# Kernel tuning notes

Hardware: AMD Instinct MI355X
Metric: run time of the kernel (lower is better)

The kernel has to match this reference:

```python
import jax, jax.numpy as jnp
import numpy as np

B, IN, UNITS, E = 32768, 1024, 1024, 8

def setup_inputs() -> dict:
    key = jax.random.key(0)
    k1, k2, k3, k4 = jax.random.split(key, 4)
    x = jax.random.normal(k1, (B, IN), dtype=jnp.float32)
    # gate percentages: soft mixing weights over experts (sum to 1 like a softmax gate)
    gate_perc = jax.nn.softmax(jax.random.normal(k2, (B, E), dtype=jnp.float32), axis=-1)
    alpha = jax.random.normal(k3, (E, IN, UNITS), dtype=jnp.float32) * 0.05  # 'random_normal' init
    beta = jax.random.normal(k4, (E, UNITS), dtype=jnp.float32) * 0.05
    return {"x": x, "gate_perc": gate_perc, "alpha": alpha, "beta": beta}

def reference(x, gate_perc, alpha, beta):
    # Original math: w[b] = sum_e gate[b,e] * alpha[e]; bias[b] = sum_e gate[b,e] * beta[e];
    #                out = x[b] @ w[b] + bias[b]
    # Algebraically identical, avoiding the (B, IN, UNITS) per-sample weight tensor:
    # out[b,u] = sum_e gate[b,e] * (x[b] @ alpha[e])[u] + (gate @ beta)[b,u]
    out = jnp.einsum('bi,eiu,be->bu', x, alpha, gate_perc, optimize=True)
    out = out + gate_perc @ beta
    return out
```

## Files before the change

### kernel.cpp

```cpp
#include <hip/hip_runtime.h>

#define BSZ   32768
#define INF   1024
#define UNITS 1024
#define NE    8

using bf16x8 = __attribute__((ext_vector_type(8))) __bf16;
using f32x4  = __attribute__((ext_vector_type(4))) float;

#define GLD_LDS16(gp, lp)                                                        \
  __builtin_amdgcn_global_load_lds((__attribute__((address_space(1))) void*)(gp),\
                                   (__attribute__((address_space(3))) void*)(lp),\
                                   16, 0, 0)

__global__ __launch_bounds__(256) void transpose_cvt(const float* __restrict__ a,
                                                     __bf16* __restrict__ at) {
  __shared__ float tile[32][33];
  const int e  = blockIdx.z;
  const int u0 = blockIdx.x * 32;
  const int i0 = blockIdx.y * 32;
  const float* src = a  + (size_t)e * (INF * UNITS);
  __bf16*      dst = at + (size_t)e * (INF * UNITS);
  const int tx = threadIdx.x & 31, ty = threadIdx.x >> 5;
#pragma unroll
  for (int r = 0; r < 32; r += 8)
    tile[ty + r][tx] = src[(size_t)(i0 + ty + r) * UNITS + (u0 + tx)];
  __syncthreads();
#pragma unroll
  for (int r = 0; r < 32; r += 8)
    dst[(size_t)(u0 + ty + r) * INF + (i0 + tx)] = (__bf16)tile[tx][ty + r];
}

__global__ __launch_bounds__(256) void cvt_x(const float* __restrict__ x,
                                             __bf16* __restrict__ xb) {
  const size_t i = ((size_t)blockIdx.x * 256 + threadIdx.x) * 8;
  f32x4 a = *(const f32x4*)(x + i);
  f32x4 b = *(const f32x4*)(x + i + 4);
  bf16x8 h;
  h[0] = (__bf16)a.x; h[1] = (__bf16)a.y; h[2] = (__bf16)a.z; h[3] = (__bf16)a.w;
  h[4] = (__bf16)b.x; h[5] = (__bf16)b.y; h[6] = (__bf16)b.z; h[7] = (__bf16)b.w;
  *(bf16x8*)(xb + i) = h;
}

__global__ __launch_bounds__(512, 2) void gemm_kernel(
    const __bf16* __restrict__ xb, const float* __restrict__ gate,
    const __bf16* __restrict__ aT, const float* __restrict__ beta,
    float* __restrict__ out) {
  __shared__ __align__(16) __bf16 lA[4][128 * 64];
  __shared__ __align__(16) __bf16 lB[4][128 * 64];
  __shared__ float lG[256 * NE];

  const int t    = threadIdx.x;
  const int wave = t >> 6;
  const int lane = t & 63;
  const int wm   = wave >> 2;
  const int wn   = wave & 3;
  const int hB   = wn >> 1;
  const int fm   = lane & 15;
  const int kq   = lane >> 4;
  const int fq   = kq * 4;
  const int sw   = fm & 7;
  const int bR   = (wn & 1) * 64 + fm;

  const int li = (blockIdx.x & 7) * 64 + (blockIdx.x >> 3);
  const int bn = (li >> 7) * 256;
  const int bm = (li & 127) * 256;

  *(f32x4*)&lG[t * 4] = *(const f32x4*)&gate[(size_t)bm * NE + t * 4];

  const int stRow   = wave * 16 + (lane >> 3);
  const int stChunk = ((lane & 7) ^ (lane >> 3)) << 3;
  const __bf16* pA  = xb + (size_t)(bm + stRow) * INF + stChunk;
  const __bf16* pB  = aT + (size_t)(bn + stRow) * INF + stChunk;

#define STAGE_A(SLOT, KT, HF)                                                   \
  do {                                                                          \
    const __bf16* s_ = pA + (size_t)(HF) * (128 * INF) + (((KT) & 15) << 6);    \
    GLD_LDS16(s_, &lA[SLOT][(wave * 16) * 64]);                                 \
    GLD_LDS16(s_ + 8 * INF, &lA[SLOT][(wave * 16 + 8) * 64]);                   \
  } while (0)

#define STAGE_B(SLOT, KT, HF)                                                   \
  do {                                                                          \
    const __bf16* s_ = pB + ((size_t)((KT) >> 4) << 20) +                       \
                       (size_t)(HF) * (128 * INF) + (((KT) & 15) << 6);         \
    GLD_LDS16(s_, &lB[SLOT][(wave * 16) * 64]);                                 \
    GLD_LDS16(s_ + 8 * INF, &lB[SLOT][(wave * 16 + 8) * 64]);                   \
  } while (0)

#define LDAF(SLOT, ROW, C) \
  (*(const bf16x8*)&lA[SLOT][((ROW) << 6) + ((((C) ^ sw)) << 3)])
#define LDBF(SLOT, ROW, C) \
  (*(const bf16x8*)&lB[SLOT][((ROW) << 6) + ((((C) ^ sw)) << 3)])

#define LOAD_B(SLOT)                                    \
  _Pragma("unroll") for (int n = 0; n < 4; ++n) {       \
    bq[n][0] = LDBF(SLOT, bR + n * 16, kq);             \
    bq[n][1] = LDBF(SLOT, bR + n * 16, 4 + kq);         \
  }

#define LOAD_A(SLOT, Q)                                        \
  _Pragma("unroll") for (int mm = 0; mm < 2; ++mm) {           \
    aq[mm][0] = LDAF(SLOT, (Q) * 32 + mm * 16 + fm, kq);       \
    aq[mm][1] = LDAF(SLOT, (Q) * 32 + mm * 16 + fm, 4 + kq);   \
  }

#define VMW(N) asm volatile("s_waitcnt vmcnt(" #N ")" ::: "memory")

#define MFMA_BLK(Q)                                                            \
  do {                                                                         \
    __builtin_amdgcn_s_barrier();                                              \
    asm volatile("s_waitcnt lgkmcnt(0)" ::: "memory");                         \
    __builtin_amdgcn_s_setprio(1);                                             \
    _Pragma("unroll") for (int mm = 0; mm < 2; ++mm)                           \
    _Pragma("unroll") for (int n = 0; n < 4; ++n) {                            \
      acc[(Q) * 2 + mm][n] = __builtin_amdgcn_mfma_f32_16x16x32_bf16(          \
          aq[mm][0], bq[n][0], acc[(Q) * 2 + mm][n], 0, 0, 0);                 \
      acc[(Q) * 2 + mm][n] = __builtin_amdgcn_mfma_f32_16x16x32_bf16(          \
          aq[mm][1], bq[n][1], acc[(Q) * 2 + mm][n], 0, 0, 0);                 \
    }                                                                          \
    __builtin_amdgcn_s_setprio(0);                                             \
    __builtin_amdgcn_s_barrier();                                              \
    asm volatile("" ::: "memory");                                             \
  } while (0)

#define RESCALE(E)                                                 \
  do {                                                             \
    _Pragma("unroll") for (int m = 0; m < 8; ++m)                  \
    _Pragma("unroll") for (int r = 0; r < 4; ++r) {                \
      const int rowL  = wm * 128 + m * 16 + fq + r;                \
      const float go  = lG[rowL * NE + (E)-1];                     \
      const float gn  = lG[rowL * NE + (E)];                       \
      const float ra  = go / gn;                                   \
      _Pragma("unroll") for (int n = 0; n < 4; ++n)                \
        acc[m][n][r] *= ra;                                        \
    }                                                              \
  } while (0)

  bf16x8 aq[2][2], bq[4][2];
  f32x4  acc[8][4] = {};

  STAGE_B(0, 0, 0); STAGE_B(1, 0, 1);
  STAGE_A(0, 0, 0); STAGE_A(1, 0, 1);
  STAGE_B(2, 1, 0); STAGE_B(3, 1, 1);
  asm volatile("s_waitcnt vmcnt(4) lgkmcnt(0)" ::: "memory");
  __builtin_amdgcn_s_barrier();
  asm volatile("" ::: "memory");

#pragma unroll 1
  for (int i = 0; i < 63; ++i) {
    if (i && !(i & 7)) RESCALE(i >> 3);
    const int kt1 = 2 * i + 1, ktn = 2 * i + 2, ktn1 = 2 * i + 3;
    LOAD_B(hB);     LOAD_A(wm, 0);     STAGE_A(2, kt1, 0);           MFMA_BLK(0);
                    LOAD_A(wm, 1);     STAGE_A(3, kt1, 1);           MFMA_BLK(1);
                    LOAD_A(wm, 2);     STAGE_B(0, ktn, 0);           MFMA_BLK(2);
                    LOAD_A(wm, 3);     STAGE_B(1, ktn, 1);  VMW(4);  MFMA_BLK(3);
    LOAD_B(2 + hB); LOAD_A(2 + wm, 0); STAGE_A(0, ktn, 0);           MFMA_BLK(0);
                    LOAD_A(2 + wm, 1); STAGE_A(1, ktn, 1);           MFMA_BLK(1);
                    LOAD_A(2 + wm, 2); STAGE_B(2, ktn1, 0);          MFMA_BLK(2);
                    LOAD_A(2 + wm, 3); STAGE_B(3, ktn1, 1); VMW(4);  MFMA_BLK(3);
  }
  {
    LOAD_B(hB);     LOAD_A(wm, 0);     STAGE_A(2, 127, 0);           MFMA_BLK(0);
                    LOAD_A(wm, 1);     STAGE_A(3, 127, 1);           MFMA_BLK(1);
                    LOAD_A(wm, 2);                                   MFMA_BLK(2);
                    LOAD_A(wm, 3);                          VMW(0);  MFMA_BLK(3);
    LOAD_B(2 + hB); LOAD_A(2 + wm, 0);                               MFMA_BLK(0);
                    LOAD_A(2 + wm, 1);                               MFMA_BLK(1);
                    LOAD_A(2 + wm, 2);                               MFMA_BLK(2);
                    LOAD_A(2 + wm, 3);                               MFMA_BLK(3);
  }

  float bcol[4][NE];
#pragma unroll
  for (int n = 0; n < 4; ++n) {
    const int u = bn + wn * 64 + n * 16 + fm;
#pragma unroll
    for (int e2 = 0; e2 < NE; ++e2) bcol[n][e2] = beta[e2 * UNITS + u];
  }
#pragma unroll
  for (int m = 0; m < 8; ++m) {
#pragma unroll
    for (int r = 0; r < 4; ++r) {
      const int rowL = wm * 128 + m * 16 + fq + r;
      const int b    = bm + rowL;
      float g8[NE];
#pragma unroll
      for (int e2 = 0; e2 < NE; ++e2) g8[e2] = lG[rowL * NE + e2];
#pragma unroll
      for (int n = 0; n < 4; ++n) {
        float bias = 0.f;
#pragma unroll
        for (int e2 = 0; e2 < NE; ++e2) bias += g8[e2] * bcol[n][e2];
        const int u = bn + wn * 64 + n * 16 + fm;
        out[(size_t)b * UNITS + u] = g8[7] * acc[m][n][r] + bias;
      }
    }
  }
}

extern "C" void kernel_launch(void* const* d_in, const int* in_sizes, int n_in,
                              void* d_out, int out_size, void* d_ws, size_t ws_size,
                              hipStream_t stream) {
  const float* x     = (const float*)d_in[0];
  const float* gate  = (const float*)d_in[1];
  const float* alpha = (const float*)d_in[2];
  const float* beta  = (const float*)d_in[3];
  float* out         = (float*)d_out;
  __bf16* aT  = (__bf16*)d_ws;
  __bf16* xbp = (__bf16*)((char*)d_ws + (size_t)16 * 1024 * 1024);

  transpose_cvt<<<dim3(UNITS / 32, INF / 32, NE), 256, 0, stream>>>(alpha, aT);
  cvt_x<<<dim3(BSZ * INF / (256 * 8)), 256, 0, stream>>>(x, xbp);
  gemm_kernel<<<dim3(512), 512, 0, stream>>>(xbp, gate, aT, beta, out);
}
```

Measured before the change: 752.3 us.

## Double-buffer MFMA operand fragments and halve barriers in the GEMM main loop

```diff
diff --git a/kernel.cpp b/kernel.cpp
--- a/kernel.cpp
+++ b/kernel.cpp
@@ -93,35 +93,35 @@
 #define LDBF(SLOT, ROW, C) \
   (*(const bf16x8*)&lB[SLOT][((ROW) << 6) + ((((C) ^ sw)) << 3)])
 
-#define LOAD_B(SLOT)                                    \
-  _Pragma("unroll") for (int n = 0; n < 4; ++n) {       \
-    bq[n][0] = LDBF(SLOT, bR + n * 16, kq);             \
-    bq[n][1] = LDBF(SLOT, bR + n * 16, 4 + kq);         \
-  }
-
-#define LOAD_A(SLOT, Q)                                        \
-  _Pragma("unroll") for (int mm = 0; mm < 2; ++mm) {           \
-    aq[mm][0] = LDAF(SLOT, (Q) * 32 + mm * 16 + fm, kq);       \
-    aq[mm][1] = LDAF(SLOT, (Q) * 32 + mm * 16 + fm, 4 + kq);   \
-  }
+#define LOAD_A_TO(DST, SLOT, Q)                                   \
+  _Pragma("unroll") for (int mm = 0; mm < 2; ++mm) {              \
+    DST[mm][0] = LDAF(SLOT, (Q) * 32 + mm * 16 + fm, kq);         \
+    DST[mm][1] = LDAF(SLOT, (Q) * 32 + mm * 16 + fm, 4 + kq);     \
+  }
+
+#define LOAD_BH(DST, SLOT, KH)                                    \
+  _Pragma("unroll") for (int n = 0; n < 4; ++n)                   \
+    DST[n][KH] = LDBF(SLOT, bR + n * 16, (KH) * 4 + kq);
 
 #define VMW(N) asm volatile("s_waitcnt vmcnt(" #N ")" ::: "memory")
 
-#define MFMA_BLK(Q)                                                            \
+#define BAR()                                  \
+  do {                                         \
+    __builtin_amdgcn_s_barrier();              \
+    asm volatile("" ::: "memory");             \
+  } while (0)
+
+#define MFMA8(AQ, BQ, Q)                                                       \
   do {                                                                         \
-    __builtin_amdgcn_s_barrier();                                              \
-    asm volatile("s_waitcnt lgkmcnt(0)" ::: "memory");                         \
     __builtin_amdgcn_s_setprio(1);                                             \
     _Pragma("unroll") for (int mm = 0; mm < 2; ++mm)                           \
     _Pragma("unroll") for (int n = 0; n < 4; ++n) {                            \
       acc[(Q) * 2 + mm][n] = __builtin_amdgcn_mfma_f32_16x16x32_bf16(          \
-          aq[mm][0], bq[n][0], acc[(Q) * 2 + mm][n], 0, 0, 0);                 \
+          AQ[mm][0], BQ[n][0], acc[(Q) * 2 + mm][n], 0, 0, 0);                 \
       acc[(Q) * 2 + mm][n] = __builtin_amdgcn_mfma_f32_16x16x32_bf16(          \
-          aq[mm][1], bq[n][1], acc[(Q) * 2 + mm][n], 0, 0, 0);                 \
+          AQ[mm][1], BQ[n][1], acc[(Q) * 2 + mm][n], 0, 0, 0);                 \
     }                                                                          \
     __builtin_amdgcn_s_setprio(0);                                             \
-    __builtin_amdgcn_s_barrier();                                              \
-    asm volatile("" ::: "memory");                                             \
   } while (0)
 
 #define RESCALE(E)                                                 \
@@ -137,38 +137,40 @@
     }                                                              \
   } while (0)
 
-  bf16x8 aq[2][2], bq[4][2];
+  bf16x8 aq0[2][2], aq1[2][2], bq0[4][2], bq1[4][2];
   f32x4  acc[8][4] = {};
 
   STAGE_B(0, 0, 0); STAGE_B(1, 0, 1);
   STAGE_A(0, 0, 0); STAGE_A(1, 0, 1);
   STAGE_B(2, 1, 0); STAGE_B(3, 1, 1);
-  asm volatile("s_waitcnt vmcnt(4) lgkmcnt(0)" ::: "memory");
-  __builtin_amdgcn_s_barrier();
-  asm volatile("" ::: "memory");
+  VMW(4);
+  asm volatile("s_waitcnt lgkmcnt(0)" ::: "memory");
+  BAR();
+  LOAD_BH(bq0, hB, 0); LOAD_BH(bq0, hB, 1);
+  LOAD_A_TO(aq0, wm, 0);
 
 #pragma unroll 1
   for (int i = 0; i < 63; ++i) {
     if (i && !(i & 7)) RESCALE(i >> 3);
     const int kt1 = 2 * i + 1, ktn = 2 * i + 2, ktn1 = 2 * i + 3;
-    LOAD_B(hB);     LOAD_A(wm, 0);     STAGE_A(2, kt1, 0);           MFMA_BLK(0);
-                    LOAD_A(wm, 1);     STAGE_A(3, kt1, 1);           MFMA_BLK(1);
-                    LOAD_A(wm, 2);     STAGE_B(0, ktn, 0);           MFMA_BLK(2);
-                    LOAD_A(wm, 3);     STAGE_B(1, ktn, 1);  VMW(4);  MFMA_BLK(3);
-    LOAD_B(2 + hB); LOAD_A(2 + wm, 0); STAGE_A(0, ktn, 0);           MFMA_BLK(0);
-                    LOAD_A(2 + wm, 1); STAGE_A(1, ktn, 1);           MFMA_BLK(1);
-                    LOAD_A(2 + wm, 2); STAGE_B(2, ktn1, 0);          MFMA_BLK(2);
-                    LOAD_A(2 + wm, 3); STAGE_B(3, ktn1, 1); VMW(4);  MFMA_BLK(3);
+    STAGE_A(2, kt1, 0);          LOAD_A_TO(aq1, wm, 1);                            MFMA8(aq0, bq0, 0); BAR();
+    STAGE_A(3, kt1, 1); VMW(4);  LOAD_A_TO(aq0, wm, 2);                            MFMA8(aq1, bq0, 1); BAR();
+    STAGE_B(0, ktn, 0);          LOAD_A_TO(aq1, wm, 3);     LOAD_BH(bq1, 2+hB, 0); MFMA8(aq0, bq0, 2); BAR();
+    STAGE_B(1, ktn, 1); VMW(4);  LOAD_BH(bq1, 2+hB, 1);     LOAD_A_TO(aq0, 2+wm, 0); MFMA8(aq1, bq0, 3); BAR();
+    STAGE_A(0, ktn, 0);          LOAD_A_TO(aq1, 2+wm, 1);                          MFMA8(aq0, bq1, 0); BAR();
+    STAGE_A(1, ktn, 1); VMW(4);  LOAD_A_TO(aq0, 2+wm, 2);                          MFMA8(aq1, bq1, 1); BAR();
+    STAGE_B(2, ktn1, 0);         LOAD_A_TO(aq1, 2+wm, 3);   LOAD_BH(bq0, hB, 0);   MFMA8(aq0, bq1, 2); BAR();
+    STAGE_B(3, ktn1, 1); VMW(4); LOAD_BH(bq0, hB, 1);       LOAD_A_TO(aq0, wm, 0); MFMA8(aq1, bq1, 3); BAR();
   }
   {
-    LOAD_B(hB);     LOAD_A(wm, 0);     STAGE_A(2, 127, 0);           MFMA_BLK(0);
-                    LOAD_A(wm, 1);     STAGE_A(3, 127, 1);           MFMA_BLK(1);
-                    LOAD_A(wm, 2);                                   MFMA_BLK(2);
-                    LOAD_A(wm, 3);                          VMW(0);  MFMA_BLK(3);
-    LOAD_B(2 + hB); LOAD_A(2 + wm, 0);                               MFMA_BLK(0);
-                    LOAD_A(2 + wm, 1);                               MFMA_BLK(1);
-                    LOAD_A(2 + wm, 2);                               MFMA_BLK(2);
-                    LOAD_A(2 + wm, 3);                               MFMA_BLK(3);
+    STAGE_A(2, 127, 0);          LOAD_A_TO(aq1, wm, 1);                            MFMA8(aq0, bq0, 0); BAR();
+    STAGE_A(3, 127, 1); VMW(4);  LOAD_A_TO(aq0, wm, 2);                            MFMA8(aq1, bq0, 1); BAR();
+                                 LOAD_A_TO(aq1, wm, 3);     LOAD_BH(bq1, 2+hB, 0); MFMA8(aq0, bq0, 2); BAR();
+    VMW(0);                      LOAD_BH(bq1, 2+hB, 1);     LOAD_A_TO(aq0, 2+wm, 0); MFMA8(aq1, bq0, 3); BAR();
+                                 LOAD_A_TO(aq1, 2+wm, 1);                          MFMA8(aq0, bq1, 0); BAR();
+                                 LOAD_A_TO(aq0, 2+wm, 2);                          MFMA8(aq1, bq1, 1); BAR();
+                                 LOAD_A_TO(aq1, 2+wm, 3);                          MFMA8(aq0, bq1, 2); BAR();
+                                                                                   MFMA8(aq1, bq1, 3);
   }
 
   float bcol[4][NE];
```

Measured after the change: 810.2 us. 7.7% more time.

## Pre-pack alpha into MFMA fragment layout and load B straight to registers

Applied to the files above, without the earlier changes.

```diff
diff --git a/kernel.cpp b/kernel.cpp
--- a/kernel.cpp
+++ b/kernel.cpp
@@ -13,22 +13,29 @@
                                    (__attribute__((address_space(3))) void*)(lp),\
                                    16, 0, 0)
 
-__global__ __launch_bounds__(256) void transpose_cvt(const float* __restrict__ a,
-                                                     __bf16* __restrict__ at) {
-  __shared__ float tile[32][33];
+__global__ __launch_bounds__(256) void pack_b(const float* __restrict__ a,
+                                              __bf16* __restrict__ pk) {
+  __shared__ float ld[64][132];
   const int e  = blockIdx.z;
-  const int u0 = blockIdx.x * 32;
-  const int i0 = blockIdx.y * 32;
-  const float* src = a  + (size_t)e * (INF * UNITS);
-  __bf16*      dst = at + (size_t)e * (INF * UNITS);
-  const int tx = threadIdx.x & 31, ty = threadIdx.x >> 5;
-#pragma unroll
-  for (int r = 0; r < 32; r += 8)
-    tile[ty + r][tx] = src[(size_t)(i0 + ty + r) * UNITS + (u0 + tx)];
+  const int kt = blockIdx.y;
+  const int ub = blockIdx.x;
+  const float* src = a + (size_t)e * (INF * UNITS) + (size_t)(kt * 64) * UNITS + ub * 128;
+  const int c = threadIdx.x & 127, r2 = threadIdx.x >> 7;
+#pragma unroll 4
+  for (int p = 0; p < 32; ++p)
+    ld[p * 2 + r2][c] = src[(size_t)(p * 2 + r2) * UNITS + c];
   __syncthreads();
-#pragma unroll
-  for (int r = 0; r < 32; r += 8)
-    dst[(size_t)(u0 + ty + r) * INF + (i0 + tx)] = (__bf16)tile[tx][ty + r];
+  const int l = threadIdx.x & 63, rl = threadIdx.x >> 6;
+  const int kq_ = l >> 4, fm_ = l & 15;
+  for (int rec = rl; rec < 16; rec += 4) {
+    const int kh = rec >> 3, n16l = rec & 7;
+    bf16x8 v;
+#pragma unroll
+    for (int j = 0; j < 8; ++j)
+      v[j] = (__bf16)ld[kh * 32 + kq_ * 8 + j][n16l * 16 + fm_];
+    const size_t R = (size_t)((e * 16 + kt) * 2 + kh) * 64 + ub * 8 + n16l;
+    *(bf16x8*)(pk + R * 512 + l * 8) = v;
+  }
 }
 
 __global__ __launch_bounds__(256) void cvt_x(const float* __restrict__ x,
@@ -44,10 +51,9 @@
 
 __global__ __launch_bounds__(512, 2) void gemm_kernel(
     const __bf16* __restrict__ xb, const float* __restrict__ gate,
-    const __bf16* __restrict__ aT, const float* __restrict__ beta,
+    const __bf16* __restrict__ pk, const float* __restrict__ beta,
     float* __restrict__ out) {
-  __shared__ __align__(16) __bf16 lA[4][128 * 64];
-  __shared__ __align__(16) __bf16 lB[4][128 * 64];
+  __shared__ __align__(16) __bf16 lA[8][128 * 64];
   __shared__ float lG[256 * NE];
 
   const int t    = threadIdx.x;
@@ -60,18 +66,18 @@
   const int kq   = lane >> 4;
   const int fq   = kq * 4;
   const int sw   = fm & 7;
-  const int bR   = (wn & 1) * 64 + fm;
+  const int lane8 = lane * 8;
 
   const int li = (blockIdx.x & 7) * 64 + (blockIdx.x >> 3);
   const int bn = (li >> 7) * 256;
   const int bm = (li & 127) * 256;
+  const int n16b = (bn >> 4) + hB * 8 + (wn & 1) * 4;
 
   *(f32x4*)&lG[t * 4] = *(const f32x4*)&gate[(size_t)bm * NE + t * 4];
 
   const int stRow   = wave * 16 + (lane >> 3);
   const int stChunk = ((lane & 7) ^ (lane >> 3)) << 3;
   const __bf16* pA  = xb + (size_t)(bm + stRow) * INF + stChunk;
-  const __bf16* pB  = aT + (size_t)(bn + stRow) * INF + stChunk;
 
 #define STAGE_A(SLOT, KT, HF)                                                   \
   do {                                                                          \
@@ -80,34 +86,21 @@
     GLD_LDS16(s_ + 8 * INF, &lA[SLOT][(wave * 16 + 8) * 64]);                   \
   } while (0)
 
-#define STAGE_B(SLOT, KT, HF)                                                   \
-  do {                                                                          \
-    const __bf16* s_ = pB + ((size_t)((KT) >> 4) << 20) +                       \
-                       (size_t)(HF) * (128 * INF) + (((KT) & 15) << 6);         \
-    GLD_LDS16(s_, &lB[SLOT][(wave * 16) * 64]);                                 \
-    GLD_LDS16(s_ + 8 * INF, &lB[SLOT][(wave * 16 + 8) * 64]);                   \
-  } while (0)
-
 #define LDAF(SLOT, ROW, C) \
   (*(const bf16x8*)&lA[SLOT][((ROW) << 6) + ((((C) ^ sw)) << 3)])
-#define LDBF(SLOT, ROW, C) \
-  (*(const bf16x8*)&lB[SLOT][((ROW) << 6) + ((((C) ^ sw)) << 3)])
-
-#define LOAD_B(SLOT)                                    \
-  _Pragma("unroll") for (int n = 0; n < 4; ++n) {       \
-    bq[n][0] = LDBF(SLOT, bR + n * 16, kq);             \
-    bq[n][1] = LDBF(SLOT, bR + n * 16, 4 + kq);         \
-  }
-
-#define LOAD_A(SLOT, Q)                                        \
-  _Pragma("unroll") for (int mm = 0; mm < 2; ++mm) {           \
-    aq[mm][0] = LDAF(SLOT, (Q) * 32 + mm * 16 + fm, kq);       \
-    aq[mm][1] = LDAF(SLOT, (Q) * 32 + mm * 16 + fm, 4 + kq);   \
-  }
-
-#define VMW(N) asm volatile("s_waitcnt vmcnt(" #N ")" ::: "memory")
-
-#define MFMA_BLK(Q)                                                            \
+
+#define DSA(PAIR, Q)                                                        \
+  _Pragma("unroll") for (int mm = 0; mm < 2; ++mm) {                        \
+    aq[mm][0] = LDAF((PAIR) * 2 + wm, (Q) * 32 + mm * 16 + fm, kq);         \
+    aq[mm][1] = LDAF((PAIR) * 2 + wm, (Q) * 32 + mm * 16 + fm, 4 + kq);     \
+  }
+
+#define LDB(DST, KT, KH)                                                    \
+  _Pragma("unroll") for (int n = 0; n < 4; ++n)                             \
+    DST[n][KH] = *(const bf16x8*)(pk +                                      \
+        ((size_t)((KT) * 2 + (KH)) * 64 + n16b + n) * 512 + lane8);
+
+#define MF(BQ, Q)                                                              \
   do {                                                                         \
     __builtin_amdgcn_s_barrier();                                              \
     asm volatile("s_waitcnt lgkmcnt(0)" ::: "memory");                         \
@@ -115,9 +108,9 @@
     _Pragma("unroll") for (int mm = 0; mm < 2; ++mm)                           \
     _Pragma("unroll") for (int n = 0; n < 4; ++n) {                            \
       acc[(Q) * 2 + mm][n] = __builtin_amdgcn_mfma_f32_16x16x32_bf16(          \
-          aq[mm][0], bq[n][0], acc[(Q) * 2 + mm][n], 0, 0, 0);                 \
+          aq[mm][0], BQ[n][0], acc[(Q) * 2 + mm][n], 0, 0, 0);                 \
       acc[(Q) * 2 + mm][n] = __builtin_amdgcn_mfma_f32_16x16x32_bf16(          \
-          aq[mm][1], bq[n][1], acc[(Q) * 2 + mm][n], 0, 0, 0);                 \
+          aq[mm][1], BQ[n][1], acc[(Q) * 2 + mm][n], 0, 0, 0);                 \
     }                                                                          \
     __builtin_amdgcn_s_setprio(0);                                             \
     __builtin_amdgcn_s_barrier();                                              \
@@ -137,38 +130,59 @@
     }                                                              \
   } while (0)
 
-  bf16x8 aq[2][2], bq[4][2];
+  bf16x8 aq[2][2], bqA[4][2], bqB[4][2];
   f32x4  acc[8][4] = {};
 
-  STAGE_B(0, 0, 0); STAGE_B(1, 0, 1);
   STAGE_A(0, 0, 0); STAGE_A(1, 0, 1);
-  STAGE_B(2, 1, 0); STAGE_B(3, 1, 1);
-  asm volatile("s_waitcnt vmcnt(4) lgkmcnt(0)" ::: "memory");
+  STAGE_A(2, 1, 0); STAGE_A(3, 1, 1);
+  STAGE_A(4, 2, 0); STAGE_A(5, 2, 1);
+  asm volatile("" ::: "memory");
+  LDB(bqA, 0, 0); LDB(bqA, 0, 1);
+  asm volatile("" ::: "memory");
+  asm volatile("s_waitcnt vmcnt(16)" ::: "memory");
+  asm volatile("s_waitcnt lgkmcnt(0)" ::: "memory");
   __builtin_amdgcn_s_barrier();
   asm volatile("" ::: "memory");
 
 #pragma unroll 1
-  for (int i = 0; i < 63; ++i) {
-    if (i && !(i & 7)) RESCALE(i >> 3);
-    const int kt1 = 2 * i + 1, ktn = 2 * i + 2, ktn1 = 2 * i + 3;
-    LOAD_B(hB);     LOAD_A(wm, 0);     STAGE_A(2, kt1, 0);           MFMA_BLK(0);
-                    LOAD_A(wm, 1);     STAGE_A(3, kt1, 1);           MFMA_BLK(1);
-                    LOAD_A(wm, 2);     STAGE_B(0, ktn, 0);           MFMA_BLK(2);
-                    LOAD_A(wm, 3);     STAGE_B(1, ktn, 1);  VMW(4);  MFMA_BLK(3);
-    LOAD_B(2 + hB); LOAD_A(2 + wm, 0); STAGE_A(0, ktn, 0);           MFMA_BLK(0);
-                    LOAD_A(2 + wm, 1); STAGE_A(1, ktn, 1);           MFMA_BLK(1);
-                    LOAD_A(2 + wm, 2); STAGE_B(2, ktn1, 0);          MFMA_BLK(2);
-                    LOAD_A(2 + wm, 3); STAGE_B(3, ktn1, 1); VMW(4);  MFMA_BLK(3);
+  for (int j = 0; j < 31; ++j) {
+    if (j && !(j & 3)) RESCALE(j >> 2);
+    const int T1 = 4 * j + 1, T2 = 4 * j + 2, T3 = 4 * j + 3;
+    const int T4 = 4 * j + 4, T5 = 4 * j + 5, T6 = 4 * j + 6;
+    DSA(0, 0); STAGE_A(6, T3, 0); LDB(bqB, T1, 0); MF(bqA, 0);
+    DSA(0, 1); STAGE_A(7, T3, 1); LDB(bqB, T1, 1); MF(bqA, 1);
+    DSA(0, 2);                                      MF(bqA, 2);
+    DSA(0, 3);                                      MF(bqA, 3);
+    DSA(1, 0); STAGE_A(0, T4, 0); LDB(bqA, T2, 0); MF(bqB, 0);
+    DSA(1, 1); STAGE_A(1, T4, 1); LDB(bqA, T2, 1); MF(bqB, 1);
+    DSA(1, 2);                                      MF(bqB, 2);
+    DSA(1, 3);                                      MF(bqB, 3);
+    DSA(2, 0); STAGE_A(2, T5, 0); LDB(bqB, T3, 0); MF(bqA, 0);
+    DSA(2, 1); STAGE_A(3, T5, 1); LDB(bqB, T3, 1); MF(bqA, 1);
+    DSA(2, 2);                                      MF(bqA, 2);
+    DSA(2, 3);                                      MF(bqA, 3);
+    DSA(3, 0); STAGE_A(4, T6, 0); LDB(bqA, T4, 0); MF(bqB, 0);
+    DSA(3, 1); STAGE_A(5, T6, 1); LDB(bqA, T4, 1); MF(bqB, 1);
+    DSA(3, 2);                                      MF(bqB, 2);
+    DSA(3, 3);                                      MF(bqB, 3);
   }
   {
-    LOAD_B(hB);     LOAD_A(wm, 0);     STAGE_A(2, 127, 0);           MFMA_BLK(0);
-                    LOAD_A(wm, 1);     STAGE_A(3, 127, 1);           MFMA_BLK(1);
-                    LOAD_A(wm, 2);                                   MFMA_BLK(2);
-                    LOAD_A(wm, 3);                          VMW(0);  MFMA_BLK(3);
-    LOAD_B(2 + hB); LOAD_A(2 + wm, 0);                               MFMA_BLK(0);
-                    LOAD_A(2 + wm, 1);                               MFMA_BLK(1);
-                    LOAD_A(2 + wm, 2);                               MFMA_BLK(2);
-                    LOAD_A(2 + wm, 3);                               MFMA_BLK(3);
+    DSA(0, 0); STAGE_A(6, 127, 0); LDB(bqB, 125, 0); MF(bqA, 0);
+    DSA(0, 1); STAGE_A(7, 127, 1); LDB(bqB, 125, 1); MF(bqA, 1);
+    DSA(0, 2);                                        MF(bqA, 2);
+    DSA(0, 3);                                        MF(bqA, 3);
+    DSA(1, 0);                     LDB(bqA, 126, 0);  MF(bqB, 0);
+    DSA(1, 1);                     LDB(bqA, 126, 1);  MF(bqB, 1);
+    DSA(1, 2);                                        MF(bqB, 2);
+    DSA(1, 3);                                        MF(bqB, 3);
+    DSA(2, 0);                     LDB(bqB, 127, 0);  MF(bqA, 0);
+    DSA(2, 1);                     LDB(bqB, 127, 1);  MF(bqA, 1);
+    DSA(2, 2);                                        MF(bqA, 2);
+    DSA(2, 3);                                        MF(bqA, 3);
+    DSA(3, 0);                                        MF(bqB, 0);
+    DSA(3, 1);                                        MF(bqB, 1);
+    DSA(3, 2);                                        MF(bqB, 2);
+    DSA(3, 3);                                        MF(bqB, 3);
   }
 
   float bcol[4][NE];
@@ -207,10 +221,10 @@
   const float* alpha = (const float*)d_in[2];
   const float* beta  = (const float*)d_in[3];
   float* out         = (float*)d_out;
-  __bf16* aT  = (__bf16*)d_ws;
+  __bf16* pk  = (__bf16*)d_ws;
   __bf16* xbp = (__bf16*)((char*)d_ws + (size_t)16 * 1024 * 1024);
 
-  transpose_cvt<<<dim3(UNITS / 32, INF / 32, NE), 256, 0, stream>>>(alpha, aT);
+  pack_b<<<dim3(8, 16, NE), 256, 0, stream>>>(alpha, pk);
   cvt_x<<<dim3(BSZ * INF / (256 * 8)), 256, 0, stream>>>(x, xbp);
-  gemm_kernel<<<dim3(512), 512, 0, stream>>>(xbp, gate, aT, beta, out);
-}
+  gemm_kernel<<<dim3(512), 512, 0, stream>>>(xbp, gate, pk, beta, out);
+}
```

Result: slower. 805.2 us (+7.0%).
